# Performance work log

Measured on AMD Instinct MI355X. Metric: run time of the kernel, lower is better.

## Reference

```python
import jax, jax.numpy as jnp
import numpy as np

N_COMBIN, N_DEV, CONT, VOCAB, EMB = 50000, 100000, 62, 1000, 16
B, K, H, OUT, NCLS = 8192, 64, 4, 16, 1
FEAT = CONT + 2 * EMB  # 94
ALPHA = 0.2  # leaky relu slope


def setup_inputs() -> dict:
    key = jax.random.key(0)
    ks = jax.random.split(key, 32)
    rn = lambda k, shape, s=0.05: (jax.random.normal(k, shape, dtype=jnp.float32) * s)
    inp = {
        "combin_cont": jax.random.normal(ks[0], (N_COMBIN, CONT), jnp.float32),
        "combin_cat": jax.random.randint(ks[1], (N_COMBIN, 2), 0, VOCAB),
        "device_cont": jax.random.normal(ks[2], (N_DEV, CONT), jnp.float32),
        "device_cat": jax.random.randint(ks[3], (N_DEV, 2), 0, VOCAB),
        "combin_idx": jax.random.randint(ks[4], (B,), 0, N_COMBIN),
        "device_idx": jax.random.randint(ks[5], (B,), 0, N_DEV),
        "neighbor_idx": jax.random.randint(ks[6], (B, K), 0, N_DEV),
        "ce0": rn(ks[7], (VOCAB, EMB), 1.0),
        "ce1": rn(ks[8], (VOCAB, EMB), 1.0),
        "de0": rn(ks[9], (VOCAB, EMB), 1.0),
        "de1": rn(ks[10], (VOCAB, EMB), 1.0),
        "Wc": rn(ks[11], (H, FEAT, OUT)),
        "bc": rn(ks[12], (H, OUT)),
        "Wd": rn(ks[13], (H, FEAT, OUT)),
        "bd": rn(ks[14], (H, OUT)),
        "aW": rn(ks[15], (H, 2 * OUT)),
        "ab": rn(ks[16], (H,)),
        "W1": rn(ks[17], (H * OUT, OUT)),
        "b1": rn(ks[18], (OUT,)),
        "W2": rn(ks[19], (OUT + 2 * FEAT, 64)),
        "b2": rn(ks[20], (64,)),
        "W3": rn(ks[21], (64, 32)),
        "b3": rn(ks[22], (32,)),
        "W4": rn(ks[23], (32, NCLS)),
        "b4": rn(ks[24], (NCLS,)),
    }
    return inp


def reference(combin_cont, combin_cat, device_cont, device_cat,
              combin_idx, device_idx, neighbor_idx,
              ce0, ce1, de0, de1,
              Wc, bc, Wd, bd, aW, ab,
              W1, b1, W2, b2, W3, b3, W4, b4):
    # concat_embed_feats for device nodes: [N_dev, FEAT]
    dev_feats = jnp.concatenate(
        [device_cont, de0[device_cat[:, 0]], de1[device_cat[:, 1]]], axis=1)
    # combin batch features: [B, FEAT]
    cc = combin_cat[combin_idx]
    comb_batch = jnp.concatenate(
        [combin_cont[combin_idx], ce0[cc[:, 0]], ce1[cc[:, 1]]], axis=1)
    dev_batch = dev_feats[device_idx]            # [B, FEAT]
    neibr = dev_feats[neighbor_idx]              # [B, K, FEAT]

    # multi-head GAT attention (all heads vectorized)
    h_c = jnp.einsum('bf,hfo->bho', comb_batch, Wc) + bc[None]          # [B,H,OUT]
    h_n = jnp.einsum('bkf,hfo->bhko', neibr, Wd) + bd[None, :, None]    # [B,H,K,OUT]
    a1, a2 = aW[:, :OUT], aW[:, OUT:]
    e = (jnp.einsum('bho,ho->bh', h_c, a1)[:, :, None]
         + jnp.einsum('bhko,ho->bhk', h_n, a2)
         + ab[None, :, None])                                           # [B,H,K]
    e = jax.nn.leaky_relu(e, negative_slope=ALPHA)
    attn = jax.nn.softmax(e, axis=-1)
    head_out = jax.nn.elu(jnp.einsum('bhk,bhko->bho', attn, h_n))       # [B,H,OUT]
    attn_feats = head_out.reshape(head_out.shape[0], H * OUT) @ W1 + b1  # [B,OUT]

    fusion = jnp.concatenate([comb_batch, dev_batch, attn_feats], axis=1)
    x = jax.nn.relu(fusion @ W2 + b2)   # dropout is identity in eval
    x = jax.nn.relu(x @ W3 + b3)
    return jax.nn.sigmoid(x @ W4 + b4)  # [B, NCLS]
```

## Files before the change

kernel.cpp:

```cpp
#include <hip/hip_runtime.h>
#include <cmath>

#define NDEV   100000
#define NBATCH 8192
#define CONTF  62
#define EMB    16
#define FEAT   94
#define KNBR   64
#define NH     4
#define OUTD   16
#define HOUT   64
#define FUS    204
#define ALPHA  0.2f

#define NDEVG2  782
#define NCOMBG2 64
#define KP      48

typedef unsigned short ushortT;
typedef unsigned int   uintT;
typedef ushortT ushort8v __attribute__((ext_vector_type(8)));
typedef short   short8  __attribute__((ext_vector_type(8)));
typedef float   float4v __attribute__((ext_vector_type(4)));


template <typename T>
__device__ __forceinline__ const T* uniform_ptr(const T* p) {
  uint64_t v = (uint64_t)(uintptr_t)p;
  uint32_t lo = __builtin_amdgcn_readfirstlane((uint32_t)v);
  uint32_t hi = __builtin_amdgcn_readfirstlane((uint32_t)(v >> 32));
  return (const T*)(uintptr_t)(((uint64_t)hi << 32) | lo);
}

__device__ __forceinline__ float bf2f(ushortT u) {
  return __uint_as_float(((unsigned int)u) << 16);
}
__device__ __forceinline__ ushortT f2bf(float f) {
  unsigned int i = __float_as_uint(f);
  unsigned int r = i + 0x7FFFu + ((i >> 16) & 1u);
  return (ushortT)(r >> 16);
}
__device__ __forceinline__ uintT pack2(float lo, float hi) {
  return ((uintT)f2bf(hi) << 16) | (uintT)f2bf(lo);
}

union FragU { uint4 u; short8 s; };

__global__ __launch_bounds__(256) void k_prep(
    const float* __restrict__ Wd, const float* __restrict__ Wc,
    uintT* __restrict__ wpack) {
  const int e = blockIdx.x * 256 + threadIdx.x;
  if (e >= 2 * 64 * KP) return;
  const bool dev = e < 64 * KP;
  const int i = dev ? e : e - 64 * KP;
  const int n = i / KP, p = i - n * KP;
  const int h = n >> 4, o = n & 15;
  const float* __restrict__ Ws = dev ? Wd : Wc;
  uintT v = 0u;
  if (p < 47) {
    const float lo = Ws[(h * FEAT + 2 * p) * OUTD + o];
    const float hi = Ws[(h * FEAT + 2 * p + 1) * OUTD + o];
    v = pack2(lo, hi);
  }
  wpack[e] = v;
}

__global__ __launch_bounds__(256, 2) void k_feat(
    const float* __restrict__ device_cont, const int* __restrict__ device_cat,
    const float* __restrict__ de0, const float* __restrict__ de1,
    const float* __restrict__ bd,
    const float* __restrict__ combin_cont, const int* __restrict__ combin_cat,
    const int* __restrict__ combin_idx,
    const float* __restrict__ ce0, const float* __restrict__ ce1,
    const float* __restrict__ bc,
    const float* __restrict__ aW, const uintT* __restrict__ wpack,
    ushortT* __restrict__ h_bf, float* __restrict__ e_d, float* __restrict__ e_c) {
  __shared__ uintT x_s[128 * KP];
  __shared__ uintT w_s[64 * KP];
  __shared__ int   ci_s[128];

  const int tid  = threadIdx.x;
  const int lane = tid & 63;
  const int wv = __builtin_amdgcn_readfirstlane((int)(tid >> 6));
  const int blk = blockIdx.x;
  const bool devp = blk < NDEVG2;
  const int b0 = (devp ? blk : blk - NDEVG2) * 128;

  if (!devp && tid < 128) ci_s[tid] = combin_idx[b0 + tid];

  {
    const uint4* __restrict__ wp =
        reinterpret_cast<const uint4*>(wpack + (devp ? 0 : 64 * KP));
#pragma unroll
    for (int t = 0; t < 3; ++t)
      reinterpret_cast<uint4*>(w_s)[t * 256 + tid] = wp[t * 256 + tid];
  }
  __syncthreads();

  {
    const float* __restrict__ cont = devp ? device_cont : combin_cont;
#pragma unroll 1
    for (int e = tid; e < 128 * 31; e += 256) {
      const int r = e / 31, p = e - r * 31;
      const size_t srow = devp ? (size_t)min(b0 + r, NDEV - 1) : (size_t)ci_s[r];
      const float2 v = *reinterpret_cast<const float2*>(cont + srow * CONTF + 2 * p);
      x_s[r * KP + p] = pack2(v.x, v.y);
    }
  }
  {
    const int r = tid >> 1, tb = tid & 1;
    const int srow = devp ? min(b0 + r, NDEV - 1) : ci_s[r];
    const int cidx = (devp ? device_cat : combin_cat)[2 * srow + tb];
    const float* __restrict__ ep =
        (tb ? (devp ? de1 : ce1) : (devp ? de0 : ce0)) + (size_t)cidx * EMB;
    uintT* __restrict__ dst = &x_s[r * KP + 31 + tb * 8];
#pragma unroll
    for (int k4 = 0; k4 < 4; ++k4) {
      const float4 v = reinterpret_cast<const float4*>(ep)[k4];
      dst[2 * k4 + 0] = pack2(v.x, v.y);
      dst[2 * k4 + 1] = pack2(v.z, v.w);
    }
  }
  if (tid < 128) x_s[tid * KP + 47] = 0u;
  __syncthreads();

  const int m = lane & 15, q = lane >> 4;
  const float* bias = uniform_ptr(devp ? bd : bc);
  const float* aWl  = uniform_ptr(aW);

  float4v acc[2][NH];
#pragma unroll
  for (int ct = 0; ct < NH; ++ct) {
    const float bv = bias[ct * OUTD + m];
    acc[0][ct] = (float4v){bv, bv, bv, bv};
    acc[1][ct] = (float4v){bv, bv, bv, bv};
  }

  const uintT* xa0 = &x_s[(wv * 16 + m) * KP + q * 4];
  const uintT* xa1 = &x_s[(64 + wv * 16 + m) * KP + q * 4];
#pragma unroll
  for (int c = 0; c < 3; ++c) {
    FragU af0, af1;
    af0.u = *reinterpret_cast<const uint4*>(xa0 + c * 16);
    af1.u = *reinterpret_cast<const uint4*>(xa1 + c * 16);
#pragma unroll
    for (int ct = 0; ct < NH; ++ct) {
      FragU bf;
      bf.u = *reinterpret_cast<const uint4*>(&w_s[(ct * 16 + m) * KP + c * 16 + q * 4]);
      acc[0][ct] = __builtin_amdgcn_mfma_f32_16x16x32_bf16(af0.s, bf.s, acc[0][ct], 0, 0, 0);
      acc[1][ct] = __builtin_amdgcn_mfma_f32_16x16x32_bf16(af1.s, bf.s, acc[1][ct], 0, 0, 0);
    }
  }

  const int aoff = devp ? OUTD : 0;
  float* __restrict__ eout = devp ? e_d : e_c;
#pragma unroll
  for (int rt = 0; rt < 2; ++rt) {
    const int rowq = b0 + rt * 64 + wv * 16 + q * 4;
#pragma unroll
    for (int ct = 0; ct < NH; ++ct) {
      const float av = aWl[ct * 2 * OUTD + aoff + m];
      float e0 = acc[rt][ct][0] * av, e1 = acc[rt][ct][1] * av,
            e2 = acc[rt][ct][2] * av, e3 = acc[rt][ct][3] * av;
#pragma unroll
      for (int msk = 1; msk < 16; msk <<= 1) {
        e0 += __shfl_xor(e0, msk);
        e1 += __shfl_xor(e1, msk);
        e2 += __shfl_xor(e2, msk);
        e3 += __shfl_xor(e3, msk);
      }
      if (m == ct) {
        const float ev[4] = {e0, e1, e2, e3};
#pragma unroll
        for (int r = 0; r < 4; ++r)
          if (!devp || rowq + r < NDEV) eout[(size_t)(rowq + r) * NH + ct] = ev[r];
      }
    }
    if (devp) {
#pragma unroll
      for (int ct = 0; ct < NH; ++ct) {
#pragma unroll
        for (int r = 0; r < 4; ++r) {
          if (rowq + r < NDEV)
            h_bf[(size_t)(rowq + r) * HOUT + ct * OUTD + m] = f2bf(acc[rt][ct][r]);
        }
      }
    }
  }
}

__global__ __launch_bounds__(256, 4) void k_attn(
    const int* __restrict__ neighbor_idx, const int* __restrict__ device_idx,
    const int* __restrict__ device_cat, const float* __restrict__ device_cont,
    const float* __restrict__ de0, const float* __restrict__ de1,
    const int* __restrict__ combin_idx, const int* __restrict__ combin_cat,
    const float* __restrict__ combin_cont,
    const float* __restrict__ ce0, const float* __restrict__ ce1,
    const ushortT* __restrict__ h_bf, const float* __restrict__ e_d,
    const float* __restrict__ e_c, const float* __restrict__ ab,
    const float* __restrict__ W1, const float* __restrict__ b1,
    const float* __restrict__ W2, const float* __restrict__ b2,
    const float* __restrict__ W3, const float* __restrict__ b3,
    const float* __restrict__ W4, const float* __restrict__ b4,
    float* __restrict__ out) {
  __shared__ __align__(16) float pb[4][NH][68];
  __shared__ __align__(16) int   nb[4][KNBR];
  __shared__ __align__(16) float hb[4][HOUT];
  __shared__ __align__(16) float fusb[4][208];
  __shared__ __align__(16) float x1b[4][64];

  const int lane = threadIdx.x & 63;
  const int wid  = __builtin_amdgcn_readfirstlane((int)(threadIdx.x >> 6));
  const int b    = blockIdx.x * 4 + wid;

  const int nk = neighbor_idx[(size_t)b * KNBR + lane];
  const float4 ed4 = *reinterpret_cast<const float4*>(e_d + (size_t)nk * NH);
  const float4 ec4 = *reinterpret_cast<const float4*>(e_c + (size_t)b * NH);
  const float4 ab4 = *reinterpret_cast<const float4*>(ab);

  float v0 = ec4.x + ed4.x + ab4.x;
  float v1 = ec4.y + ed4.y + ab4.y;
  float v2 = ec4.z + ed4.z + ab4.z;
  float v3 = ec4.w + ed4.w + ab4.w;
  v0 = v0 > 0.f ? v0 : ALPHA * v0;
  v1 = v1 > 0.f ? v1 : ALPHA * v1;
  v2 = v2 > 0.f ? v2 : ALPHA * v2;
  v3 = v3 > 0.f ? v3 : ALPHA * v3;

  float m0 = v0, m1 = v1, m2 = v2, m3 = v3;
#pragma unroll
  for (int msk = 1; msk < 64; msk <<= 1) {
    m0 = fmaxf(m0, __shfl_xor(m0, msk));
    m1 = fmaxf(m1, __shfl_xor(m1, msk));
    m2 = fmaxf(m2, __shfl_xor(m2, msk));
    m3 = fmaxf(m3, __shfl_xor(m3, msk));
  }
  float p0 = expf(v0 - m0), p1 = expf(v1 - m1), p2 = expf(v2 - m2), p3 = expf(v3 - m3);
  float s0 = p0, s1 = p1, s2 = p2, s3 = p3;
#pragma unroll
  for (int msk = 1; msk < 64; msk <<= 1) {
    s0 += __shfl_xor(s0, msk);
    s1 += __shfl_xor(s1, msk);
    s2 += __shfl_xor(s2, msk);
    s3 += __shfl_xor(s3, msk);
  }
  p0 /= s0; p1 /= s1; p2 /= s2; p3 /= s3;

  pb[wid][0][lane] = p0;
  pb[wid][1][lane] = p1;
  pb[wid][2][lane] = p2;
  pb[wid][3][lane] = p3;
  nb[wid][lane]    = nk;

  const int ci = combin_idx[b];
  const int cc0 = combin_cat[2 * ci], cc1 = combin_cat[2 * ci + 1];
  const int didx = device_idx[b];
  const int dc0 = device_cat[2 * didx], dc1 = device_cat[2 * didx + 1];
#pragma unroll
  for (int t = 0; t < 3; ++t) {
    const int i = lane + t * 64;
    if (i < 188) {
      float v;
      if (i < 62)       v = combin_cont[(size_t)ci * CONTF + i];
      else if (i < 78)  v = ce0[(size_t)cc0 * EMB + (i - 62)];
      else if (i < 94)  v = ce1[(size_t)cc1 * EMB + (i - 78)];
      else if (i < 156) v = device_cont[(size_t)didx * CONTF + (i - 94)];
      else if (i < 172) v = de0[(size_t)dc0 * EMB + (i - 156)];
      else              v = de1[(size_t)dc1 * EMB + (i - 172)];
      fusb[wid][i] = v;
    }
  }
  __builtin_amdgcn_wave_barrier();

  {
    const int q = lane >> 3, c8 = lane & 7;
    const int hq = c8 >> 1;
    float a[8];
#pragma unroll
    for (int i = 0; i < 8; ++i) a[i] = 0.f;
#pragma unroll
    for (int t = 0; t < 8; ++t) {
      const int k   = q * 8 + t;
      const int n   = nb[wid][k];
      const float p = pb[wid][hq][k];
      const ushort8v hv =
          *reinterpret_cast<const ushort8v*>(h_bf + (size_t)n * HOUT + c8 * 8);
#pragma unroll
      for (int i = 0; i < 8; ++i) a[i] = fmaf(p, bf2f(hv[i]), a[i]);
    }
#pragma unroll
    for (int msk = 8; msk < 64; msk <<= 1) {
#pragma unroll
      for (int i = 0; i < 8; ++i) a[i] += __shfl_xor(a[i], msk);
    }
    if (q == 0) {
#pragma unroll
      for (int i = 0; i < 8; ++i) a[i] = a[i] > 0.f ? a[i] : expm1f(a[i]);
      float4* hp = reinterpret_cast<float4*>(&hb[wid][c8 * 8]);
      hp[0] = make_float4(a[0], a[1], a[2], a[3]);
      hp[1] = make_float4(a[4], a[5], a[6], a[7]);
    }
  }
  __builtin_amdgcn_wave_barrier();

  {
    const int j = lane & 15, gg = lane >> 4;
    float part = 0.f;
#pragma unroll
    for (int t = 0; t < 16; ++t)
      part = fmaf(hb[wid][gg * 16 + t], W1[(gg * 16 + t) * OUTD + j], part);
    part += __shfl_xor(part, 16);
    part += __shfl_xor(part, 32);
    if (lane < 16) fusb[wid][188 + lane] = part + b1[lane];
  }
  __builtin_amdgcn_wave_barrier();

  float acc = b2[lane];
#pragma unroll 4
  for (int f = 0; f < FUS; ++f)
    acc = fmaf(fusb[wid][f], W2[f * 64 + lane], acc);
  x1b[wid][lane] = fmaxf(acc, 0.f);
  __builtin_amdgcn_wave_barrier();

  const int m = lane & 31, rh = lane >> 5;
  float x2 = rh ? 0.f : b3[m];
#pragma unroll 4
  for (int j = 0; j < 32; ++j) {
    const int jj = rh * 32 + j;
    x2 = fmaf(x1b[wid][jj], W3[jj * 32 + m], x2);
  }
  x2 += __shfl_xor(x2, 32);
  float pL3 = fmaxf(x2, 0.f) * W4[m];
#pragma unroll
  for (int msk = 1; msk < 32; msk <<= 1) pL3 += __shfl_xor(pL3, msk);
  if (lane == 0) {
    const float z = pL3 + b4[0];
    out[b] = 1.f / (1.f + expf(-z));
  }
}

extern "C" void kernel_launch(void* const* d_in, const int* in_sizes, int n_in,
                              void* d_out, int out_size, void* d_ws, size_t ws_size,
                              hipStream_t stream) {
  const float* combin_cont  = (const float*)d_in[0];
  const int*   combin_cat   = (const int*)d_in[1];
  const float* device_cont  = (const float*)d_in[2];
  const int*   device_cat   = (const int*)d_in[3];
  const int*   combin_idx   = (const int*)d_in[4];
  const int*   device_idx   = (const int*)d_in[5];
  const int*   neighbor_idx = (const int*)d_in[6];
  const float* ce0 = (const float*)d_in[7];
  const float* ce1 = (const float*)d_in[8];
  const float* de0 = (const float*)d_in[9];
  const float* de1 = (const float*)d_in[10];
  const float* Wc  = (const float*)d_in[11];
  const float* bc  = (const float*)d_in[12];
  const float* Wd  = (const float*)d_in[13];
  const float* bd  = (const float*)d_in[14];
  const float* aW  = (const float*)d_in[15];
  const float* ab  = (const float*)d_in[16];
  const float* W1  = (const float*)d_in[17];
  const float* b1  = (const float*)d_in[18];
  const float* W2  = (const float*)d_in[19];
  const float* b2  = (const float*)d_in[20];
  const float* W3  = (const float*)d_in[21];
  const float* b3  = (const float*)d_in[22];
  const float* W4  = (const float*)d_in[23];
  const float* b4  = (const float*)d_in[24];

  float* ws  = (float*)d_ws;
  ushortT* h_bf = (ushortT*)ws;
  float* e_d = ws + 3200000;
  float* e_c = ws + 3600000;
  uintT* wpack = (uintT*)(ws + 3632768);

  k_prep<<<24, 256, 0, stream>>>(Wd, Wc, wpack);
  k_feat<<<NDEVG2 + NCOMBG2, 256, 0, stream>>>(
      device_cont, device_cat, de0, de1, bd,
      combin_cont, combin_cat, combin_idx, ce0, ce1, bc, aW, wpack,
      h_bf, e_d, e_c);
  k_attn<<<2048, 256, 0, stream>>>(
      neighbor_idx, device_idx, device_cat, device_cont, de0, de1,
      combin_idx, combin_cat, combin_cont, ce0, ce1,
      h_bf, e_d, e_c, ab, W1, b1, W2, b2, W3, b3, W4, b4, (float*)d_out);
}
```

Before: 166.6 us.

## Fold weight packing into k_feat and process two rows per wave with W2 in LDS

Removes the separate k_prep launch: each k_feat block now packs Wd/Wc to bf16 straight into shared memory. k_attn now handles two batch rows per wave (8 rows per block, 1024 blocks) and stages W2 in shared memory so each weight read is reused across both rows, and W1/W3/W4 loads are shared too. In exchange, every k_feat block repeats strided weight packing, and k_attn uses about 60KB of shared memory with lower occupancy (launch bounds 2).

```diff
diff --git a/kernel.cpp b/kernel.cpp
--- a/kernel.cpp
+++ b/kernel.cpp
@@ -46,25 +46,6 @@
 
 union FragU { uint4 u; short8 s; };
 
-__global__ __launch_bounds__(256) void k_prep(
-    const float* __restrict__ Wd, const float* __restrict__ Wc,
-    uintT* __restrict__ wpack) {
-  const int e = blockIdx.x * 256 + threadIdx.x;
-  if (e >= 2 * 64 * KP) return;
-  const bool dev = e < 64 * KP;
-  const int i = dev ? e : e - 64 * KP;
-  const int n = i / KP, p = i - n * KP;
-  const int h = n >> 4, o = n & 15;
-  const float* __restrict__ Ws = dev ? Wd : Wc;
-  uintT v = 0u;
-  if (p < 47) {
-    const float lo = Ws[(h * FEAT + 2 * p) * OUTD + o];
-    const float hi = Ws[(h * FEAT + 2 * p + 1) * OUTD + o];
-    v = pack2(lo, hi);
-  }
-  wpack[e] = v;
-}
-
 __global__ __launch_bounds__(256, 2) void k_feat(
     const float* __restrict__ device_cont, const int* __restrict__ device_cat,
     const float* __restrict__ de0, const float* __restrict__ de1,
@@ -73,7 +54,8 @@
     const int* __restrict__ combin_idx,
     const float* __restrict__ ce0, const float* __restrict__ ce1,
     const float* __restrict__ bc,
-    const float* __restrict__ aW, const uintT* __restrict__ wpack,
+    const float* __restrict__ aW,
+    const float* __restrict__ Wd, const float* __restrict__ Wc,
     ushortT* __restrict__ h_bf, float* __restrict__ e_d, float* __restrict__ e_c) {
   __shared__ uintT x_s[128 * KP];
   __shared__ uintT w_s[64 * KP];
@@ -89,11 +71,20 @@
   if (!devp && tid < 128) ci_s[tid] = combin_idx[b0 + tid];
 
   {
-    const uint4* __restrict__ wp =
-        reinterpret_cast<const uint4*>(wpack + (devp ? 0 : 64 * KP));
-#pragma unroll
-    for (int t = 0; t < 3; ++t)
-      reinterpret_cast<uint4*>(w_s)[t * 256 + tid] = wp[t * 256 + tid];
+    const float* __restrict__ Ws = devp ? Wd : Wc;
+#pragma unroll
+    for (int t = 0; t < 12; ++t) {
+      const int e = t * 256 + tid;
+      const int n = e / KP, p = e - n * KP;
+      const int h = n >> 4, o = n & 15;
+      uintT v = 0u;
+      if (p < 47) {
+        const float lo = Ws[(h * FEAT + 2 * p) * OUTD + o];
+        const float hi = Ws[(h * FEAT + 2 * p + 1) * OUTD + o];
+        v = pack2(lo, hi);
+      }
+      w_s[e] = v;
+    }
   }
   __syncthreads();
 
@@ -189,7 +180,7 @@
   }
 }
 
-__global__ __launch_bounds__(256, 4) void k_attn(
+__global__ __launch_bounds__(256, 2) void k_attn(
     const int* __restrict__ neighbor_idx, const int* __restrict__ device_idx,
     const int* __restrict__ device_cat, const float* __restrict__ device_cont,
     const float* __restrict__ de0, const float* __restrict__ de1,
@@ -203,71 +194,94 @@
     const float* __restrict__ W3, const float* __restrict__ b3,
     const float* __restrict__ W4, const float* __restrict__ b4,
     float* __restrict__ out) {
-  __shared__ __align__(16) float pb[4][NH][68];
-  __shared__ __align__(16) int   nb[4][KNBR];
-  __shared__ __align__(16) float hb[4][HOUT];
-  __shared__ __align__(16) float fusb[4][208];
-  __shared__ __align__(16) float x1b[4][64];
-
-  const int lane = threadIdx.x & 63;
-  const int wid  = __builtin_amdgcn_readfirstlane((int)(threadIdx.x >> 6));
-  const int b    = blockIdx.x * 4 + wid;
-
-  const int nk = neighbor_idx[(size_t)b * KNBR + lane];
-  const float4 ed4 = *reinterpret_cast<const float4*>(e_d + (size_t)nk * NH);
-  const float4 ec4 = *reinterpret_cast<const float4*>(e_c + (size_t)b * NH);
+  __shared__ __align__(16) float w2s[FUS * 64];
+  __shared__ __align__(16) float pb[8][NH][68];
+  __shared__ __align__(16) int   nb[8][KNBR];
+  __shared__ __align__(16) float hb[8][HOUT];
+  __shared__ __align__(16) float fusb[8][208];
+  __shared__ __align__(16) float x1b[8][64];
+
+  const int tid  = threadIdx.x;
+  const int lane = tid & 63;
+  const int wid  = __builtin_amdgcn_readfirstlane((int)(tid >> 6));
+  const int rbase = blockIdx.x * 8 + wid * 2;
+  const int rl0 = wid * 2, rl1 = rl0 + 1;
+
+  {
+    const float4* __restrict__ src = reinterpret_cast<const float4*>(W2);
+    float4* __restrict__ dst = reinterpret_cast<float4*>(w2s);
+#pragma unroll
+    for (int t = 0; t < 13; ++t) {
+      const int i = t * 256 + tid;
+      if (i < (FUS * 64) / 4) dst[i] = src[i];
+    }
+  }
+
   const float4 ab4 = *reinterpret_cast<const float4*>(ab);
-
-  float v0 = ec4.x + ed4.x + ab4.x;
-  float v1 = ec4.y + ed4.y + ab4.y;
-  float v2 = ec4.z + ed4.z + ab4.z;
-  float v3 = ec4.w + ed4.w + ab4.w;
-  v0 = v0 > 0.f ? v0 : ALPHA * v0;
-  v1 = v1 > 0.f ? v1 : ALPHA * v1;
-  v2 = v2 > 0.f ? v2 : ALPHA * v2;
-  v3 = v3 > 0.f ? v3 : ALPHA * v3;
-
-  float m0 = v0, m1 = v1, m2 = v2, m3 = v3;
-#pragma unroll
-  for (int msk = 1; msk < 64; msk <<= 1) {
-    m0 = fmaxf(m0, __shfl_xor(m0, msk));
-    m1 = fmaxf(m1, __shfl_xor(m1, msk));
-    m2 = fmaxf(m2, __shfl_xor(m2, msk));
-    m3 = fmaxf(m3, __shfl_xor(m3, msk));
-  }
-  float p0 = expf(v0 - m0), p1 = expf(v1 - m1), p2 = expf(v2 - m2), p3 = expf(v3 - m3);
-  float s0 = p0, s1 = p1, s2 = p2, s3 = p3;
-#pragma unroll
-  for (int msk = 1; msk < 64; msk <<= 1) {
-    s0 += __shfl_xor(s0, msk);
-    s1 += __shfl_xor(s1, msk);
-    s2 += __shfl_xor(s2, msk);
-    s3 += __shfl_xor(s3, msk);
-  }
-  p0 /= s0; p1 /= s1; p2 /= s2; p3 /= s3;
-
-  pb[wid][0][lane] = p0;
-  pb[wid][1][lane] = p1;
-  pb[wid][2][lane] = p2;
-  pb[wid][3][lane] = p3;
-  nb[wid][lane]    = nk;
-
-  const int ci = combin_idx[b];
-  const int cc0 = combin_cat[2 * ci], cc1 = combin_cat[2 * ci + 1];
-  const int didx = device_idx[b];
-  const int dc0 = device_cat[2 * didx], dc1 = device_cat[2 * didx + 1];
-#pragma unroll
-  for (int t = 0; t < 3; ++t) {
-    const int i = lane + t * 64;
-    if (i < 188) {
-      float v;
-      if (i < 62)       v = combin_cont[(size_t)ci * CONTF + i];
-      else if (i < 78)  v = ce0[(size_t)cc0 * EMB + (i - 62)];
-      else if (i < 94)  v = ce1[(size_t)cc1 * EMB + (i - 78)];
-      else if (i < 156) v = device_cont[(size_t)didx * CONTF + (i - 94)];
-      else if (i < 172) v = de0[(size_t)dc0 * EMB + (i - 156)];
-      else              v = de1[(size_t)dc1 * EMB + (i - 172)];
-      fusb[wid][i] = v;
+#pragma unroll
+  for (int r2 = 0; r2 < 2; ++r2) {
+    const int b  = rbase + r2;
+    const int rl = rl0 + r2;
+    const int nk = neighbor_idx[(size_t)b * KNBR + lane];
+    const float4 ed4 = *reinterpret_cast<const float4*>(e_d + (size_t)nk * NH);
+    const float4 ec4 = *reinterpret_cast<const float4*>(e_c + (size_t)b * NH);
+
+    float v0 = ec4.x + ed4.x + ab4.x;
+    float v1 = ec4.y + ed4.y + ab4.y;
+    float v2 = ec4.z + ed4.z + ab4.z;
+    float v3 = ec4.w + ed4.w + ab4.w;
+    v0 = v0 > 0.f ? v0 : ALPHA * v0;
+    v1 = v1 > 0.f ? v1 : ALPHA * v1;
+    v2 = v2 > 0.f ? v2 : ALPHA * v2;
+    v3 = v3 > 0.f ? v3 : ALPHA * v3;
+
+    float m0 = v0, m1 = v1, m2 = v2, m3 = v3;
+#pragma unroll
+    for (int msk = 1; msk < 64; msk <<= 1) {
+      m0 = fmaxf(m0, __shfl_xor(m0, msk));
+      m1 = fmaxf(m1, __shfl_xor(m1, msk));
+      m2 = fmaxf(m2, __shfl_xor(m2, msk));
+      m3 = fmaxf(m3, __shfl_xor(m3, msk));
+    }
+    float p0 = expf(v0 - m0), p1 = expf(v1 - m1), p2 = expf(v2 - m2), p3 = expf(v3 - m3);
+    float s0 = p0, s1 = p1, s2 = p2, s3 = p3;
+#pragma unroll
+    for (int msk = 1; msk < 64; msk <<= 1) {
+      s0 += __shfl_xor(s0, msk);
+      s1 += __shfl_xor(s1, msk);
+      s2 += __shfl_xor(s2, msk);
+      s3 += __shfl_xor(s3, msk);
+    }
+    p0 /= s0; p1 /= s1; p2 /= s2; p3 /= s3;
+
+    pb[rl][0][lane] = p0;
+    pb[rl][1][lane] = p1;
+    pb[rl][2][lane] = p2;
+    pb[rl][3][lane] = p3;
+    nb[rl][lane]    = nk;
+  }
+
+#pragma unroll
+  for (int r2 = 0; r2 < 2; ++r2) {
+    const int b  = rbase + r2;
+    const int rl = rl0 + r2;
+    const int ci = combin_idx[b];
+    const int cc0 = combin_cat[2 * ci], cc1 = combin_cat[2 * ci + 1];
+    const int didx = device_idx[b];
+    const int dc0 = device_cat[2 * didx], dc1 = device_cat[2 * didx + 1];
+#pragma unroll
+    for (int t = 0; t < 3; ++t) {
+      const int i = lane + t * 64;
+      if (i < 188) {
+        float v;
+        if (i < 62)       v = combin_cont[(size_t)ci * CONTF + i];
+        else if (i < 78)  v = ce0[(size_t)cc0 * EMB + (i - 62)];
+        else if (i < 94)  v = ce1[(size_t)cc1 * EMB + (i - 78)];
+        else if (i < 156) v = device_cont[(size_t)didx * CONTF + (i - 94)];
+        else if (i < 172) v = de0[(size_t)dc0 * EMB + (i - 156)];
+        else              v = de1[(size_t)dc1 * EMB + (i - 172)];
+        fusb[rl][i] = v;
+      }
     }
   }
   __builtin_amdgcn_wave_barrier();
@@ -275,67 +289,109 @@
   {
     const int q = lane >> 3, c8 = lane & 7;
     const int hq = c8 >> 1;
-    float a[8];
-#pragma unroll
-    for (int i = 0; i < 8; ++i) a[i] = 0.f;
+    float a0[8], a1[8];
+#pragma unroll
+    for (int i = 0; i < 8; ++i) { a0[i] = 0.f; a1[i] = 0.f; }
 #pragma unroll
     for (int t = 0; t < 8; ++t) {
-      const int k   = q * 8 + t;
-      const int n   = nb[wid][k];
-      const float p = pb[wid][hq][k];
-      const ushort8v hv =
-          *reinterpret_cast<const ushort8v*>(h_bf + (size_t)n * HOUT + c8 * 8);
-#pragma unroll
-      for (int i = 0; i < 8; ++i) a[i] = fmaf(p, bf2f(hv[i]), a[i]);
+      const int k = q * 8 + t;
+      const int n0 = nb[rl0][k], n1 = nb[rl1][k];
+      const float p0 = pb[rl0][hq][k], p1 = pb[rl1][hq][k];
+      const ushort8v h0 =
+          *reinterpret_cast<const ushort8v*>(h_bf + (size_t)n0 * HOUT + c8 * 8);
+      const ushort8v h1 =
+          *reinterpret_cast<const ushort8v*>(h_bf + (size_t)n1 * HOUT + c8 * 8);
+#pragma unroll
+      for (int i = 0; i < 8; ++i) {
+        a0[i] = fmaf(p0, bf2f(h0[i]), a0[i]);
+        a1[i] = fmaf(p1, bf2f(h1[i]), a1[i]);
+      }
     }
 #pragma unroll
     for (int msk = 8; msk < 64; msk <<= 1) {
 #pragma unroll
-      for (int i = 0; i < 8; ++i) a[i] += __shfl_xor(a[i], msk);
+      for (int i = 0; i < 8; ++i) {
+        a0[i] += __shfl_xor(a0[i], msk);
+        a1[i] += __shfl_xor(a1[i], msk);
+      }
     }
     if (q == 0) {
 #pragma unroll
-      for (int i = 0; i < 8; ++i) a[i] = a[i] > 0.f ? a[i] : expm1f(a[i]);
-      float4* hp = reinterpret_cast<float4*>(&hb[wid][c8 * 8]);
-      hp[0] = make_float4(a[0], a[1], a[2], a[3]);
-      hp[1] = make_float4(a[4], a[5], a[6], a[7]);
+      for (int i = 0; i < 8; ++i) {
+        a0[i] = a0[i] > 0.f ? a0[i] : expm1f(a0[i]);
+        a1[i] = a1[i] > 0.f ? a1[i] : expm1f(a1[i]);
+      }
+      float4* hp0 = reinterpret_cast<float4*>(&hb[rl0][c8 * 8]);
+      hp0[0] = make_float4(a0[0], a0[1], a0[2], a0[3]);
+      hp0[1] = make_float4(a0[4], a0[5], a0[6], a0[7]);
+      float4* hp1 = reinterpret_cast<float4*>(&hb[rl1][c8 * 8]);
+      hp1[0] = make_float4(a1[0], a1[1], a1[2], a1[3]);
+      hp1[1] = make_float4(a1[4], a1[5], a1[6], a1[7]);
     }
   }
   __builtin_amdgcn_wave_barrier();
 
   {
     const int j = lane & 15, gg = lane >> 4;
-    float part = 0.f;
-#pragma unroll
-    for (int t = 0; t < 16; ++t)
-      part = fmaf(hb[wid][gg * 16 + t], W1[(gg * 16 + t) * OUTD + j], part);
-    part += __shfl_xor(part, 16);
-    part += __shfl_xor(part, 32);
-    if (lane < 16) fusb[wid][188 + lane] = part + b1[lane];
+    float pa = 0.f, pc = 0.f;
+#pragma unroll
+    for (int t = 0; t < 16; ++t) {
+      const float w = W1[(gg * 16 + t) * OUTD + j];
+      pa = fmaf(hb[rl0][gg * 16 + t], w, pa);
+      pc = fmaf(hb[rl1][gg * 16 + t], w, pc);
+    }
+    pa += __shfl_xor(pa, 16);
+    pa += __shfl_xor(pa, 32);
+    pc += __shfl_xor(pc, 16);
+    pc += __shfl_xor(pc, 32);
+    if (lane < 16) {
+      const float bb = b1[lane];
+      fusb[rl0][188 + lane] = pa + bb;
+      fusb[rl1][188 + lane] = pc + bb;
+    }
   }
   __builtin_amdgcn_wave_barrier();
-
-  float acc = b2[lane];
+  __syncthreads();
+
+  float acc0 = b2[lane];
+  float acc1 = acc0;
 #pragma unroll 4
-  for (int f = 0; f < FUS; ++f)
-    acc = fmaf(fusb[wid][f], W2[f * 64 + lane], acc);
-  x1b[wid][lane] = fmaxf(acc, 0.f);
+  for (int f2 = 0; f2 < FUS / 2; ++f2) {
+    const float2 u0 = *reinterpret_cast<const float2*>(&fusb[rl0][2 * f2]);
+    const float2 u1 = *reinterpret_cast<const float2*>(&fusb[rl1][2 * f2]);
+    const float wa = w2s[f2 * 128 + lane];
+    const float wb = w2s[f2 * 128 + 64 + lane];
+    acc0 = fmaf(u0.y, wb, fmaf(u0.x, wa, acc0));
+    acc1 = fmaf(u1.y, wb, fmaf(u1.x, wa, acc1));
+  }
+  x1b[rl0][lane] = fmaxf(acc0, 0.f);
+  x1b[rl1][lane] = fmaxf(acc1, 0.f);
   __builtin_amdgcn_wave_barrier();
 
   const int m = lane & 31, rh = lane >> 5;
-  float x2 = rh ? 0.f : b3[m];
+  float x20 = rh ? 0.f : b3[m];
+  float x21 = x20;
 #pragma unroll 4
   for (int j = 0; j < 32; ++j) {
     const int jj = rh * 32 + j;
-    x2 = fmaf(x1b[wid][jj], W3[jj * 32 + m], x2);
-  }
-  x2 += __shfl_xor(x2, 32);
-  float pL3 = fmaxf(x2, 0.f) * W4[m];
-#pragma unroll
-  for (int msk = 1; msk < 32; msk <<= 1) pL3 += __shfl_xor(pL3, msk);
+    const float w = W3[jj * 32 + m];
+    x20 = fmaf(x1b[rl0][jj], w, x20);
+    x21 = fmaf(x1b[rl1][jj], w, x21);
+  }
+  x20 += __shfl_xor(x20, 32);
+  x21 += __shfl_xor(x21, 32);
+  const float w4 = W4[m];
+  float pL0 = fmaxf(x20, 0.f) * w4;
+  float pL1 = fmaxf(x21, 0.f) * w4;
+#pragma unroll
+  for (int msk = 1; msk < 32; msk <<= 1) {
+    pL0 += __shfl_xor(pL0, msk);
+    pL1 += __shfl_xor(pL1, msk);
+  }
   if (lane == 0) {
-    const float z = pL3 + b4[0];
-    out[b] = 1.f / (1.f + expf(-z));
+    const float bz = b4[0];
+    out[rbase]     = 1.f / (1.f + expf(-(pL0 + bz)));
+    out[rbase + 1] = 1.f / (1.f + expf(-(pL1 + bz)));
   }
 }
 
@@ -372,14 +428,12 @@
   ushortT* h_bf = (ushortT*)ws;
   float* e_d = ws + 3200000;
   float* e_c = ws + 3600000;
-  uintT* wpack = (uintT*)(ws + 3632768);
-
-  k_prep<<<24, 256, 0, stream>>>(Wd, Wc, wpack);
+
   k_feat<<<NDEVG2 + NCOMBG2, 256, 0, stream>>>(
       device_cont, device_cat, de0, de1, bd,
-      combin_cont, combin_cat, combin_idx, ce0, ce1, bc, aW, wpack,
+      combin_cont, combin_cat, combin_idx, ce0, ce1, bc, aW, Wd, Wc,
       h_bf, e_d, e_c);
-  k_attn<<<2048, 256, 0, stream>>>(
+  k_attn<<<NBATCH / 8, 256, 0, stream>>>(
       neighbor_idx, device_idx, device_cat, device_cont, de0, de1,
       combin_idx, combin_cat, combin_cont, ce0, ce1,
       h_bf, e_d, e_c, ab, W1, b1, W2, b2, W3, b3, W4, b4, (float*)d_out);
```

Result: slower. 183.0 us (+9.9%).

## Fold weight packing into k_feat, prefetch neighbor rows, drop softmax max

Applied to the files above, without the earlier changes.

Removes the separate k_prep launch by having each k_feat block pack Wd/Wc into bf16 directly in shared memory. In k_attn, neighbor h rows are gathered into registers early using shuffled indices, so the gather overlaps the softmax and fusion-feature loads, and the LDS index buffer is gone. The softmax max-reduction is dropped, which saves shuffles but risks overflow in expf if attention logits are large. Each k_feat block now does redundant strided weight reads, and the prefetch adds register pressure.

```diff
diff --git a/kernel.cpp b/kernel.cpp
--- a/kernel.cpp
+++ b/kernel.cpp
@@ -46,25 +46,6 @@
 
 union FragU { uint4 u; short8 s; };
 
-__global__ __launch_bounds__(256) void k_prep(
-    const float* __restrict__ Wd, const float* __restrict__ Wc,
-    uintT* __restrict__ wpack) {
-  const int e = blockIdx.x * 256 + threadIdx.x;
-  if (e >= 2 * 64 * KP) return;
-  const bool dev = e < 64 * KP;
-  const int i = dev ? e : e - 64 * KP;
-  const int n = i / KP, p = i - n * KP;
-  const int h = n >> 4, o = n & 15;
-  const float* __restrict__ Ws = dev ? Wd : Wc;
-  uintT v = 0u;
-  if (p < 47) {
-    const float lo = Ws[(h * FEAT + 2 * p) * OUTD + o];
-    const float hi = Ws[(h * FEAT + 2 * p + 1) * OUTD + o];
-    v = pack2(lo, hi);
-  }
-  wpack[e] = v;
-}
-
 __global__ __launch_bounds__(256, 2) void k_feat(
     const float* __restrict__ device_cont, const int* __restrict__ device_cat,
     const float* __restrict__ de0, const float* __restrict__ de1,
@@ -73,7 +54,8 @@
     const int* __restrict__ combin_idx,
     const float* __restrict__ ce0, const float* __restrict__ ce1,
     const float* __restrict__ bc,
-    const float* __restrict__ aW, const uintT* __restrict__ wpack,
+    const float* __restrict__ aW,
+    const float* __restrict__ Wd, const float* __restrict__ Wc,
     ushortT* __restrict__ h_bf, float* __restrict__ e_d, float* __restrict__ e_c) {
   __shared__ uintT x_s[128 * KP];
   __shared__ uintT w_s[64 * KP];
@@ -89,11 +71,20 @@
   if (!devp && tid < 128) ci_s[tid] = combin_idx[b0 + tid];
 
   {
-    const uint4* __restrict__ wp =
-        reinterpret_cast<const uint4*>(wpack + (devp ? 0 : 64 * KP));
-#pragma unroll
-    for (int t = 0; t < 3; ++t)
-      reinterpret_cast<uint4*>(w_s)[t * 256 + tid] = wp[t * 256 + tid];
+    const float* __restrict__ Ws = devp ? Wd : Wc;
+#pragma unroll
+    for (int t = 0; t < 12; ++t) {
+      const int e = t * 256 + tid;
+      const int n = e / KP, p = e - n * KP;
+      const int h = n >> 4, o = n & 15;
+      uintT v = 0u;
+      if (p < 47) {
+        const float lo = Ws[(h * FEAT + 2 * p) * OUTD + o];
+        const float hi = Ws[(h * FEAT + 2 * p + 1) * OUTD + o];
+        v = pack2(lo, hi);
+      }
+      w_s[e] = v;
+    }
   }
   __syncthreads();
 
@@ -204,7 +195,6 @@
     const float* __restrict__ W4, const float* __restrict__ b4,
     float* __restrict__ out) {
   __shared__ __align__(16) float pb[4][NH][68];
-  __shared__ __align__(16) int   nb[4][KNBR];
   __shared__ __align__(16) float hb[4][HOUT];
   __shared__ __align__(16) float fusb[4][208];
   __shared__ __align__(16) float x1b[4][64];
@@ -218,39 +208,13 @@
   const float4 ec4 = *reinterpret_cast<const float4*>(e_c + (size_t)b * NH);
   const float4 ab4 = *reinterpret_cast<const float4*>(ab);
 
-  float v0 = ec4.x + ed4.x + ab4.x;
-  float v1 = ec4.y + ed4.y + ab4.y;
-  float v2 = ec4.z + ed4.z + ab4.z;
-  float v3 = ec4.w + ed4.w + ab4.w;
-  v0 = v0 > 0.f ? v0 : ALPHA * v0;
-  v1 = v1 > 0.f ? v1 : ALPHA * v1;
-  v2 = v2 > 0.f ? v2 : ALPHA * v2;
-  v3 = v3 > 0.f ? v3 : ALPHA * v3;
-
-  float m0 = v0, m1 = v1, m2 = v2, m3 = v3;
-#pragma unroll
-  for (int msk = 1; msk < 64; msk <<= 1) {
-    m0 = fmaxf(m0, __shfl_xor(m0, msk));
-    m1 = fmaxf(m1, __shfl_xor(m1, msk));
-    m2 = fmaxf(m2, __shfl_xor(m2, msk));
-    m3 = fmaxf(m3, __shfl_xor(m3, msk));
-  }
-  float p0 = expf(v0 - m0), p1 = expf(v1 - m1), p2 = expf(v2 - m2), p3 = expf(v3 - m3);
-  float s0 = p0, s1 = p1, s2 = p2, s3 = p3;
-#pragma unroll
-  for (int msk = 1; msk < 64; msk <<= 1) {
-    s0 += __shfl_xor(s0, msk);
-    s1 += __shfl_xor(s1, msk);
-    s2 += __shfl_xor(s2, msk);
-    s3 += __shfl_xor(s3, msk);
-  }
-  p0 /= s0; p1 /= s1; p2 /= s2; p3 /= s3;
-
-  pb[wid][0][lane] = p0;
-  pb[wid][1][lane] = p1;
-  pb[wid][2][lane] = p2;
-  pb[wid][3][lane] = p3;
-  nb[wid][lane]    = nk;
+  const int q = lane >> 3, c8 = lane & 7;
+  ushort8v hpre[8];
+#pragma unroll
+  for (int t = 0; t < 8; ++t) {
+    const int nt = __shfl(nk, q * 8 + t);
+    hpre[t] = *reinterpret_cast<const ushort8v*>(h_bf + (size_t)nt * HOUT + c8 * 8);
+  }
 
   const int ci = combin_idx[b];
   const int cc0 = combin_cat[2 * ci], cc1 = combin_cat[2 * ci + 1];
@@ -270,23 +234,43 @@
       fusb[wid][i] = v;
     }
   }
+
+  float v0 = ec4.x + ed4.x + ab4.x;
+  float v1 = ec4.y + ed4.y + ab4.y;
+  float v2 = ec4.z + ed4.z + ab4.z;
+  float v3 = ec4.w + ed4.w + ab4.w;
+  v0 = v0 > 0.f ? v0 : ALPHA * v0;
+  v1 = v1 > 0.f ? v1 : ALPHA * v1;
+  v2 = v2 > 0.f ? v2 : ALPHA * v2;
+  v3 = v3 > 0.f ? v3 : ALPHA * v3;
+
+  float p0 = expf(v0), p1 = expf(v1), p2 = expf(v2), p3 = expf(v3);
+  float s0 = p0, s1 = p1, s2 = p2, s3 = p3;
+#pragma unroll
+  for (int msk = 1; msk < 64; msk <<= 1) {
+    s0 += __shfl_xor(s0, msk);
+    s1 += __shfl_xor(s1, msk);
+    s2 += __shfl_xor(s2, msk);
+    s3 += __shfl_xor(s3, msk);
+  }
+  p0 /= s0; p1 /= s1; p2 /= s2; p3 /= s3;
+
+  pb[wid][0][lane] = p0;
+  pb[wid][1][lane] = p1;
+  pb[wid][2][lane] = p2;
+  pb[wid][3][lane] = p3;
   __builtin_amdgcn_wave_barrier();
 
   {
-    const int q = lane >> 3, c8 = lane & 7;
     const int hq = c8 >> 1;
     float a[8];
 #pragma unroll
     for (int i = 0; i < 8; ++i) a[i] = 0.f;
 #pragma unroll
     for (int t = 0; t < 8; ++t) {
-      const int k   = q * 8 + t;
-      const int n   = nb[wid][k];
-      const float p = pb[wid][hq][k];
-      const ushort8v hv =
-          *reinterpret_cast<const ushort8v*>(h_bf + (size_t)n * HOUT + c8 * 8);
-#pragma unroll
-      for (int i = 0; i < 8; ++i) a[i] = fmaf(p, bf2f(hv[i]), a[i]);
+      const float p = pb[wid][hq][q * 8 + t];
+#pragma unroll
+      for (int i = 0; i < 8; ++i) a[i] = fmaf(p, bf2f(hpre[t][i]), a[i]);
     }
 #pragma unroll
     for (int msk = 8; msk < 64; msk <<= 1) {
@@ -372,12 +356,10 @@
   ushortT* h_bf = (ushortT*)ws;
   float* e_d = ws + 3200000;
   float* e_c = ws + 3600000;
-  uintT* wpack = (uintT*)(ws + 3632768);
-
-  k_prep<<<24, 256, 0, stream>>>(Wd, Wc, wpack);
+
   k_feat<<<NDEVG2 + NCOMBG2, 256, 0, stream>>>(
       device_cont, device_cat, de0, de1, bd,
-      combin_cont, combin_cat, combin_idx, ce0, ce1, bc, aW, wpack,
+      combin_cont, combin_cat, combin_idx, ce0, ce1, bc, aW, Wd, Wc,
       h_bf, e_d, e_c);
   k_attn<<<2048, 256, 0, stream>>>(
       neighbor_idx, device_idx, device_cat, device_cont, de0, de1,
```

After: 176.2 us. +5.8%, slower.
